# Kernel optimization log

Hardware: AMD Instinct MI355X
Metric: run time of the kernel (lower is better)

## Reference

```python
import jax, jax.numpy as jnp
import numpy as np

TEMPERATURE = 1.0

def _logic_layer(x, sel_a, sel_b, gate_logits, temp):
    # x: [B, in], sel_a/sel_b: [n, in], gate_logits: [n, 16]
    a = jax.nn.softmax(sel_a / temp, axis=-1)
    b = jax.nn.softmax(sel_b / temp, axis=-1)
    p = jnp.einsum('bi,ni->bn', x, a)  # first soft operand  [B, n]
    q = jnp.einsum('bi,ni->bn', x, b)  # second soft operand [B, n]
    pq = p * q
    one = jnp.ones_like(p)
    zero = jnp.zeros_like(p)
    # 16 two-input probabilistic logic gates (difflogic ordering)
    gates = jnp.stack([
        zero,               # FALSE
        pq,                 # AND
        p - pq,             # A AND NOT B
        p,                  # A
        q - pq,             # NOT A AND B
        q,                  # B
        p + q - 2 * pq,     # XOR
        p + q - pq,         # OR
        one - (p + q - pq), # NOR
        one - (p + q - 2 * pq),  # XNOR
        one - q,            # NOT B
        one - q + pq,       # A OR NOT B
        one - p,            # NOT A
        one - p + pq,       # NOT A OR B
        one - pq,           # NAND
        one,                # TRUE
    ], axis=-1)  # [B, n, 16]
    w = jax.nn.softmax(gate_logits / temp, axis=-1)  # [n, 16]
    return jnp.einsum('bng,ng->bn', gates, w)


def setup_inputs() -> dict:
    key = jax.random.key(0)
    ks = jax.random.split(key, 13)
    B = 1048576  # 1024x1024 CA grid, flattened cells
    inp = {'x': jax.random.uniform(ks[0], (B, 9), dtype=jnp.float32)}
    dims = [(8, 9), (4, 8), (2, 4), (1, 2)]
    i = 1
    for li, (n, d) in enumerate(dims, start=1):
        inp[f'sa{li}'] = jax.random.normal(ks[i], (n, d), dtype=jnp.float32); i += 1
        inp[f'sb{li}'] = jax.random.normal(ks[i], (n, d), dtype=jnp.float32); i += 1
        inp[f'g{li}'] = jax.random.normal(ks[i], (n, 16), dtype=jnp.float32); i += 1
    return inp


def reference(x, sa1, sb1, g1, sa2, sb2, g2, sa3, sb3, g3, sa4, sb4, g4):
    t = TEMPERATURE
    h = _logic_layer(x, sa1, sb1, g1, t)   # [B, 8]
    h = _logic_layer(h, sa2, sb2, g2, t)   # [B, 4]
    h = _logic_layer(h, sa3, sb3, g3, t)   # [B, 2]
    h = _logic_layer(h, sa4, sb4, g4, t)   # [B, 1]
    return h
```

## Files before the change

### kernel.cpp

```cpp
#include <hip/hip_runtime.h>
#include <math.h>


#define THREADS 256
#define SPT 4
#define B_PER_BLOCK (THREADS * SPT)

template <int D>
__device__ __forceinline__ void softmax_row(const float* __restrict__ src,
                                            float* __restrict__ dst) {
    float e[D];
    float m = src[0];
    #pragma unroll
    for (int i = 1; i < D; ++i) m = fmaxf(m, src[i]);
    float s = 0.f;
    #pragma unroll
    for (int i = 0; i < D; ++i) { e[i] = __expf(src[i] - m); s += e[i]; }
    float inv = 1.f / s;
    #pragma unroll
    for (int i = 0; i < D; ++i) dst[i] = e[i] * inv;
}

__device__ __forceinline__ void gate_fold(const float* __restrict__ g,
                                          float* __restrict__ C) {
    const float k0[16]  = {0,0,0,0, 0,0,0,0, 1, 1, 1, 1, 1, 1, 1, 1};
    const float kp[16]  = {0,0,1,1, 0,0,1,1,-1,-1, 0, 0,-1,-1, 0, 0};
    const float kq[16]  = {0,0,0,0, 1,1,1,1,-1,-1,-1,-1, 0, 0, 0, 0};
    const float kpq[16] = {0,1,-1,0,-1,0,-2,-1, 1, 2, 0, 1, 0, 1,-1, 0};
    float w[16];
    float m = g[0];
    #pragma unroll
    for (int i = 1; i < 16; ++i) m = fmaxf(m, g[i]);
    float s = 0.f;
    #pragma unroll
    for (int i = 0; i < 16; ++i) { w[i] = __expf(g[i] - m); s += w[i]; }
    float inv = 1.f / s;
    float c0 = 0, c1 = 0, c2 = 0, c3 = 0;
    #pragma unroll
    for (int i = 0; i < 16; ++i) {
        float wi = w[i] * inv;
        c0 = fmaf(wi, k0[i], c0); c1 = fmaf(wi, kp[i], c1);
        c2 = fmaf(wi, kq[i], c2); c3 = fmaf(wi, kpq[i], c3);
    }
    C[0] = c0; C[1] = c1; C[2] = c2; C[3] = c3;
}

__global__ void coeff_kernel(const float* __restrict__ sa1, const float* __restrict__ sb1, const float* __restrict__ g1,
                             const float* __restrict__ sa2, const float* __restrict__ sb2, const float* __restrict__ g2,
                             const float* __restrict__ sa3, const float* __restrict__ sb3, const float* __restrict__ g3,
                             const float* __restrict__ sa4, const float* __restrict__ sb4, const float* __restrict__ g4,
                             float* __restrict__ cf) {
    int t = threadIdx.x;
    if (t < 8) {
        int j = t;
        softmax_row<9>(sa1 + j * 9, cf + j * 9);
        softmax_row<9>(sb1 + j * 9, cf + 72 + j * 9);
        gate_fold(g1 + j * 16, cf + 144 + j * 4);
    } else if (t < 12) {
        int j = t - 8;
        softmax_row<8>(sa2 + j * 8, cf + 176 + j * 8);
        softmax_row<8>(sb2 + j * 8, cf + 208 + j * 8);
        gate_fold(g2 + j * 16, cf + 240 + j * 4);
    } else if (t < 14) {
        int j = t - 12;
        softmax_row<4>(sa3 + j * 4, cf + 256 + j * 4);
        softmax_row<4>(sb3 + j * 4, cf + 264 + j * 4);
        gate_fold(g3 + j * 16, cf + 272 + j * 4);
    } else if (t == 14) {
        softmax_row<2>(sa4, cf + 280);
        softmax_row<2>(sb4, cf + 282);
        gate_fold(g4, cf + 284);
    }
}

__global__ __launch_bounds__(THREADS, 3) void net_kernel(
        const float* __restrict__ x, const float* __restrict__ cf,
        float* __restrict__ out, int nB) {
    const int T  = blockIdx.x * THREADS + threadIdx.x;
    const int b0 = T * SPT;
    if (b0 >= nB) return;

    float v[SPT][9];
    if (b0 + SPT <= nB) {
        const float4* __restrict__ x4 = (const float4*)x;
        float4 r[9];
        #pragma unroll
        for (int k = 0; k < 9; ++k) r[k] = x4[(long)T * 9 + k];
        const float* rf = (const float*)r;
        #pragma unroll
        for (int s = 0; s < SPT; ++s)
            #pragma unroll
            for (int i = 0; i < 9; ++i) v[s][i] = rf[s * 9 + i];
    } else {
        #pragma unroll
        for (int s = 0; s < SPT; ++s)
            #pragma unroll
            for (int i = 0; i < 9; ++i) {
                int b = b0 + s;
                v[s][i] = (b < nB) ? x[(long)b * 9 + i] : 0.f;
            }
    }

    float h1[SPT][8];
    #pragma unroll
    for (int j = 0; j < 8; ++j) {
        #pragma unroll
        for (int s = 0; s < SPT; ++s) {
            float p = 0.f, q = 0.f;
            #pragma unroll
            for (int i = 0; i < 9; ++i) {
                p = fmaf(v[s][i], cf[     j * 9 + i], p);
                q = fmaf(v[s][i], cf[72 + j * 9 + i], q);
            }
            h1[s][j] = fmaf(cf[144 + j*4 + 3], p * q,
                       fmaf(cf[144 + j*4 + 2], q,
                       fmaf(cf[144 + j*4 + 1], p, cf[144 + j*4 + 0])));
        }
    }
    float h2[SPT][4];
    #pragma unroll
    for (int j = 0; j < 4; ++j) {
        #pragma unroll
        for (int s = 0; s < SPT; ++s) {
            float p = 0.f, q = 0.f;
            #pragma unroll
            for (int i = 0; i < 8; ++i) {
                p = fmaf(h1[s][i], cf[176 + j * 8 + i], p);
                q = fmaf(h1[s][i], cf[208 + j * 8 + i], q);
            }
            h2[s][j] = fmaf(cf[240 + j*4 + 3], p * q,
                       fmaf(cf[240 + j*4 + 2], q,
                       fmaf(cf[240 + j*4 + 1], p, cf[240 + j*4 + 0])));
        }
    }
    float h3[SPT][2];
    #pragma unroll
    for (int j = 0; j < 2; ++j) {
        #pragma unroll
        for (int s = 0; s < SPT; ++s) {
            float p = 0.f, q = 0.f;
            #pragma unroll
            for (int i = 0; i < 4; ++i) {
                p = fmaf(h2[s][i], cf[256 + j * 4 + i], p);
                q = fmaf(h2[s][i], cf[264 + j * 4 + i], q);
            }
            h3[s][j] = fmaf(cf[272 + j*4 + 3], p * q,
                       fmaf(cf[272 + j*4 + 2], q,
                       fmaf(cf[272 + j*4 + 1], p, cf[272 + j*4 + 0])));
        }
    }
    float o[SPT];
    #pragma unroll
    for (int s = 0; s < SPT; ++s) {
        float p = fmaf(h3[s][0], cf[280], h3[s][1] * cf[281]);
        float q = fmaf(h3[s][0], cf[282], h3[s][1] * cf[283]);
        o[s] = fmaf(cf[287], p * q,
               fmaf(cf[286], q,
               fmaf(cf[285], p, cf[284])));
    }
    if (b0 + SPT <= nB) {
        float4* __restrict__ out4 = (float4*)out;
        float4 w; w.x = o[0]; w.y = o[1]; w.z = o[2]; w.w = o[3];
        out4[T] = w;
    } else {
        #pragma unroll
        for (int s = 0; s < SPT; ++s)
            if (b0 + s < nB) out[b0 + s] = o[s];
    }
}

extern "C" void kernel_launch(void* const* d_in, const int* in_sizes, int n_in,
                              void* d_out, int out_size, void* d_ws, size_t ws_size,
                              hipStream_t stream) {
    const float* x   = (const float*)d_in[0];
    const float* sa1 = (const float*)d_in[1];
    const float* sb1 = (const float*)d_in[2];
    const float* g1  = (const float*)d_in[3];
    const float* sa2 = (const float*)d_in[4];
    const float* sb2 = (const float*)d_in[5];
    const float* g2  = (const float*)d_in[6];
    const float* sa3 = (const float*)d_in[7];
    const float* sb3 = (const float*)d_in[8];
    const float* g3  = (const float*)d_in[9];
    const float* sa4 = (const float*)d_in[10];
    const float* sb4 = (const float*)d_in[11];
    const float* g4  = (const float*)d_in[12];
    float* cf = (float*)d_ws;
    const int nB = in_sizes[0] / 9;

    coeff_kernel<<<1, 64, 0, stream>>>(sa1, sb1, g1, sa2, sb2, g2,
                                       sa3, sb3, g3, sa4, sb4, g4, cf);
    const int grid = (nB + B_PER_BLOCK - 1) / B_PER_BLOCK;
    net_kernel<<<grid, THREADS, 0, stream>>>(x, cf, (float*)d_out, nB);
}
```

Baseline: 107.6 us.

## Stage input tile through LDS for coalesced loads and strided sample mapping

The main kernel now loads each block's input tile into shared memory with fully coalesced float4 reads, then has each thread read 4 samples strided by the block width. The results are written back through shared memory so the output store stays a coalesced float4 write. Before, each thread loaded 9 consecutive float4s, so neighbouring lanes' accesses were 144 bytes apart. The change adds 36 KB of LDS per block and two extra barriers, which may limit occupancy. The coefficient kernel is also rebalanced so that more threads each compute one softmax row.

Result: slower. 113.6 us (+5.5%).

```diff
diff --git a/kernel.cpp b/kernel.cpp
--- a/kernel.cpp
+++ b/kernel.cpp
@@ -50,55 +50,62 @@
                              const float* __restrict__ sa3, const float* __restrict__ sb3, const float* __restrict__ g3,
                              const float* __restrict__ sa4, const float* __restrict__ sb4, const float* __restrict__ g4,
                              float* __restrict__ cf) {
-    int t = threadIdx.x;
-    if (t < 8) {
-        int j = t;
-        softmax_row<9>(sa1 + j * 9, cf + j * 9);
-        softmax_row<9>(sb1 + j * 9, cf + 72 + j * 9);
-        gate_fold(g1 + j * 16, cf + 144 + j * 4);
-    } else if (t < 12) {
-        int j = t - 8;
-        softmax_row<8>(sa2 + j * 8, cf + 176 + j * 8);
-        softmax_row<8>(sb2 + j * 8, cf + 208 + j * 8);
-        gate_fold(g2 + j * 16, cf + 240 + j * 4);
-    } else if (t < 14) {
-        int j = t - 12;
-        softmax_row<4>(sa3 + j * 4, cf + 256 + j * 4);
-        softmax_row<4>(sb3 + j * 4, cf + 264 + j * 4);
-        gate_fold(g3 + j * 16, cf + 272 + j * 4);
-    } else if (t == 14) {
-        softmax_row<2>(sa4, cf + 280);
-        softmax_row<2>(sb4, cf + 282);
-        gate_fold(g4, cf + 284);
+    const int t = threadIdx.x;
+    if (t < 15) {
+        int r = t;
+        if      (r < 8)  softmax_row<9>(sa1 + r * 9,        cf + r * 9);
+        else if (r < 12) softmax_row<8>(sa2 + (r - 8) * 8,  cf + 176 + (r - 8) * 8);
+        else if (r < 14) softmax_row<4>(sa3 + (r - 12) * 4, cf + 256 + (r - 12) * 4);
+        else             softmax_row<2>(sa4,                cf + 280);
+    } else if (t >= 16 && t < 31) {
+        int r = t - 16;
+        if      (r < 8)  softmax_row<9>(sb1 + r * 9,        cf + 72 + r * 9);
+        else if (r < 12) softmax_row<8>(sb2 + (r - 8) * 8,  cf + 208 + (r - 8) * 8);
+        else if (r < 14) softmax_row<4>(sb3 + (r - 12) * 4, cf + 264 + (r - 12) * 4);
+        else             softmax_row<2>(sb4,                cf + 282);
+    } else if (t >= 32 && t < 47) {
+        int r = t - 32;
+        if      (r < 8)  gate_fold(g1 + r * 16,        cf + 144 + r * 4);
+        else if (r < 12) gate_fold(g2 + (r - 8) * 16,  cf + 240 + (r - 8) * 4);
+        else if (r < 14) gate_fold(g3 + (r - 12) * 16, cf + 272 + (r - 12) * 4);
+        else             gate_fold(g4,                 cf + 284);
     }
 }
 
 __global__ __launch_bounds__(THREADS, 3) void net_kernel(
         const float* __restrict__ x, const float* __restrict__ cf,
         float* __restrict__ out, int nB) {
-    const int T  = blockIdx.x * THREADS + threadIdx.x;
-    const int b0 = T * SPT;
-    if (b0 >= nB) return;
+    __shared__ float sx[B_PER_BLOCK * 9];
+    const int t = threadIdx.x;
+    const int blockBase = blockIdx.x * B_PER_BLOCK;
+    const int total  = nB * 9;
+    const int f4base = blockBase * 9 / 4;
+
+    const float4* __restrict__ x4 = (const float4*)x;
+    float4* sx4 = (float4*)sx;
+    #pragma unroll
+    for (int k = 0; k < 9; ++k) {
+        int idx = t + k * THREADS;
+        int fi  = f4base + idx;
+        int e   = fi * 4;
+        if (e + 3 < total) {
+            sx4[idx] = x4[fi];
+        } else {
+            float4 vv = {0.f, 0.f, 0.f, 0.f};
+            if (e     < total) vv.x = x[e];
+            if (e + 1 < total) vv.y = x[e + 1];
+            if (e + 2 < total) vv.z = x[e + 2];
+            sx4[idx] = vv;
+        }
+    }
+    __syncthreads();
 
     float v[SPT][9];
-    if (b0 + SPT <= nB) {
-        const float4* __restrict__ x4 = (const float4*)x;
-        float4 r[9];
-        #pragma unroll
-        for (int k = 0; k < 9; ++k) r[k] = x4[(long)T * 9 + k];
-        const float* rf = (const float*)r;
-        #pragma unroll
-        for (int s = 0; s < SPT; ++s)
-            #pragma unroll
-            for (int i = 0; i < 9; ++i) v[s][i] = rf[s * 9 + i];
-    } else {
-        #pragma unroll
-        for (int s = 0; s < SPT; ++s)
-            #pragma unroll
-            for (int i = 0; i < 9; ++i) {
-                int b = b0 + s;
-                v[s][i] = (b < nB) ? x[(long)b * 9 + i] : 0.f;
-            }
+    #pragma unroll
+    for (int s = 0; s < SPT; ++s) {
+        const int r = s * THREADS + t;
+        #pragma unroll
+        for (int i = 0; i < 9; ++i) v[s][i] = sx[r * 9 + i];
     }
 
     float h1[SPT][8];
@@ -158,14 +165,19 @@
                fmaf(cf[286], q,
                fmaf(cf[285], p, cf[284])));
     }
+    const int b0 = blockBase + t * SPT;
+    __syncthreads();
+    #pragma unroll
+    for (int s = 0; s < SPT; ++s) sx[s * THREADS + t] = o[s];
+    __syncthreads();
     if (b0 + SPT <= nB) {
         float4* __restrict__ out4 = (float4*)out;
-        float4 w; w.x = o[0]; w.y = o[1]; w.z = o[2]; w.w = o[3];
-        out4[T] = w;
+        const float4* __restrict__ sxo = (const float4*)sx;
+        out4[blockBase / SPT + t] = sxo[t];
     } else {
         #pragma unroll
         for (int s = 0; s < SPT; ++s)
-            if (b0 + s < nB) out[b0 + s] = o[s];
+            if (b0 + s < nB) out[b0 + s] = sx[t * SPT + s];
     }
 }
 
```

## Fold coefficient softmax kernel into main kernel via shared memory

Applied to the files above, without the earlier changes.

Removes the separate single-block coefficient kernel and its workspace round-trip. Each wave of the main kernel now computes the softmaxed selector rows and folded gate coefficients into shared memory, then reads them from LDS instead of global memory. It also splits the first layer's loop into two chunks with a compiler memory barrier, likely to limit register pressure. In exchange, every wave redoes the exponentials, and the code has no __syncthreads, so it relies on wave-synchronous LDS visibility. Uniform LDS reads may also cost more than the scalar global loads they replace.

Result: slower. 144.5 us (+34.3%).

```diff
diff --git a/kernel.cpp b/kernel.cpp
--- a/kernel.cpp
+++ b/kernel.cpp
@@ -45,38 +45,39 @@
     C[0] = c0; C[1] = c1; C[2] = c2; C[3] = c3;
 }
 
-__global__ void coeff_kernel(const float* __restrict__ sa1, const float* __restrict__ sb1, const float* __restrict__ g1,
-                             const float* __restrict__ sa2, const float* __restrict__ sb2, const float* __restrict__ g2,
-                             const float* __restrict__ sa3, const float* __restrict__ sb3, const float* __restrict__ g3,
-                             const float* __restrict__ sa4, const float* __restrict__ sb4, const float* __restrict__ g4,
-                             float* __restrict__ cf) {
-    int t = threadIdx.x;
-    if (t < 8) {
-        int j = t;
-        softmax_row<9>(sa1 + j * 9, cf + j * 9);
-        softmax_row<9>(sb1 + j * 9, cf + 72 + j * 9);
-        gate_fold(g1 + j * 16, cf + 144 + j * 4);
-    } else if (t < 12) {
-        int j = t - 8;
-        softmax_row<8>(sa2 + j * 8, cf + 176 + j * 8);
-        softmax_row<8>(sb2 + j * 8, cf + 208 + j * 8);
-        gate_fold(g2 + j * 16, cf + 240 + j * 4);
-    } else if (t < 14) {
-        int j = t - 12;
-        softmax_row<4>(sa3 + j * 4, cf + 256 + j * 4);
-        softmax_row<4>(sb3 + j * 4, cf + 264 + j * 4);
-        gate_fold(g3 + j * 16, cf + 272 + j * 4);
-    } else if (t == 14) {
-        softmax_row<2>(sa4, cf + 280);
-        softmax_row<2>(sb4, cf + 282);
-        gate_fold(g4, cf + 284);
-    }
-}
-
 __global__ __launch_bounds__(THREADS, 3) void net_kernel(
-        const float* __restrict__ x, const float* __restrict__ cf,
+        const float* __restrict__ x,
+        const float* __restrict__ sa1, const float* __restrict__ sb1, const float* __restrict__ g1,
+        const float* __restrict__ sa2, const float* __restrict__ sb2, const float* __restrict__ g2,
+        const float* __restrict__ sa3, const float* __restrict__ sb3, const float* __restrict__ g3,
+        const float* __restrict__ sa4, const float* __restrict__ sb4, const float* __restrict__ g4,
         float* __restrict__ out, int nB) {
-    const int T  = blockIdx.x * THREADS + threadIdx.x;
+    __shared__ float scf[288];
+
+    const int t    = threadIdx.x;
+    const int lane = t & 63;
+
+    if (lane < 15) {
+        int r = lane;
+        if      (r < 8)  softmax_row<9>(sa1 + r * 9,        scf + r * 9);
+        else if (r < 12) softmax_row<8>(sa2 + (r - 8) * 8,  scf + 176 + (r - 8) * 8);
+        else if (r < 14) softmax_row<4>(sa3 + (r - 12) * 4, scf + 256 + (r - 12) * 4);
+        else             softmax_row<2>(sa4,                scf + 280);
+    } else if (lane >= 16 && lane < 31) {
+        int r = lane - 16;
+        if      (r < 8)  softmax_row<9>(sb1 + r * 9,        scf + 72 + r * 9);
+        else if (r < 12) softmax_row<8>(sb2 + (r - 8) * 8,  scf + 208 + (r - 8) * 8);
+        else if (r < 14) softmax_row<4>(sb3 + (r - 12) * 4, scf + 264 + (r - 12) * 4);
+        else             softmax_row<2>(sb4,                scf + 282);
+    } else if (lane >= 32 && lane < 47) {
+        int r = lane - 32;
+        if      (r < 8)  gate_fold(g1 + r * 16,        scf + 144 + r * 4);
+        else if (r < 12) gate_fold(g2 + (r - 8) * 16,  scf + 240 + (r - 8) * 4);
+        else if (r < 14) gate_fold(g3 + (r - 12) * 16, scf + 272 + (r - 12) * 4);
+        else             gate_fold(g4,                 scf + 284);
+    }
+
+    const int T  = blockIdx.x * THREADS + t;
     const int b0 = T * SPT;
     if (b0 >= nB) return;
 
@@ -103,60 +104,65 @@
 
     float h1[SPT][8];
     #pragma unroll
-    for (int j = 0; j < 8; ++j) {
+    for (int jc = 0; jc < 2; ++jc) {
+        #pragma unroll
+        for (int jj = 0; jj < 4; ++jj) {
+            const int j = jc * 4 + jj;
+            #pragma unroll
+            for (int s = 0; s < SPT; ++s) {
+                float p = 0.f, q = 0.f;
+                #pragma unroll
+                for (int i = 0; i < 9; ++i) {
+                    p = fmaf(v[s][i], scf[     j * 9 + i], p);
+                    q = fmaf(v[s][i], scf[72 + j * 9 + i], q);
+                }
+                h1[s][j] = fmaf(scf[144 + j*4 + 3], p * q,
+                           fmaf(scf[144 + j*4 + 2], q,
+                           fmaf(scf[144 + j*4 + 1], p, scf[144 + j*4 + 0])));
+            }
+        }
+        asm volatile("" ::: "memory");
+    }
+    float h2[SPT][4];
+    #pragma unroll
+    for (int j = 0; j < 4; ++j) {
         #pragma unroll
         for (int s = 0; s < SPT; ++s) {
             float p = 0.f, q = 0.f;
             #pragma unroll
-            for (int i = 0; i < 9; ++i) {
-                p = fmaf(v[s][i], cf[     j * 9 + i], p);
-                q = fmaf(v[s][i], cf[72 + j * 9 + i], q);
-            }
-            h1[s][j] = fmaf(cf[144 + j*4 + 3], p * q,
-                       fmaf(cf[144 + j*4 + 2], q,
-                       fmaf(cf[144 + j*4 + 1], p, cf[144 + j*4 + 0])));
+            for (int i = 0; i < 8; ++i) {
+                p = fmaf(h1[s][i], scf[176 + j * 8 + i], p);
+                q = fmaf(h1[s][i], scf[208 + j * 8 + i], q);
+            }
+            h2[s][j] = fmaf(scf[240 + j*4 + 3], p * q,
+                       fmaf(scf[240 + j*4 + 2], q,
+                       fmaf(scf[240 + j*4 + 1], p, scf[240 + j*4 + 0])));
         }
     }
-    float h2[SPT][4];
-    #pragma unroll
-    for (int j = 0; j < 4; ++j) {
+    float h3[SPT][2];
+    #pragma unroll
+    for (int j = 0; j < 2; ++j) {
         #pragma unroll
         for (int s = 0; s < SPT; ++s) {
             float p = 0.f, q = 0.f;
             #pragma unroll
-            for (int i = 0; i < 8; ++i) {
-                p = fmaf(h1[s][i], cf[176 + j * 8 + i], p);
-                q = fmaf(h1[s][i], cf[208 + j * 8 + i], q);
-            }
-            h2[s][j] = fmaf(cf[240 + j*4 + 3], p * q,
-                       fmaf(cf[240 + j*4 + 2], q,
-                       fmaf(cf[240 + j*4 + 1], p, cf[240 + j*4 + 0])));
+            for (int i = 0; i < 4; ++i) {
+                p = fmaf(h2[s][i], scf[256 + j * 4 + i], p);
+                q = fmaf(h2[s][i], scf[264 + j * 4 + i], q);
+            }
+            h3[s][j] = fmaf(scf[272 + j*4 + 3], p * q,
+                       fmaf(scf[272 + j*4 + 2], q,
+                       fmaf(scf[272 + j*4 + 1], p, scf[272 + j*4 + 0])));
         }
     }
-    float h3[SPT][2];
-    #pragma unroll
-    for (int j = 0; j < 2; ++j) {
-        #pragma unroll
-        for (int s = 0; s < SPT; ++s) {
-            float p = 0.f, q = 0.f;
-            #pragma unroll
-            for (int i = 0; i < 4; ++i) {
-                p = fmaf(h2[s][i], cf[256 + j * 4 + i], p);
-                q = fmaf(h2[s][i], cf[264 + j * 4 + i], q);
-            }
-            h3[s][j] = fmaf(cf[272 + j*4 + 3], p * q,
-                       fmaf(cf[272 + j*4 + 2], q,
-                       fmaf(cf[272 + j*4 + 1], p, cf[272 + j*4 + 0])));
-        }
-    }
     float o[SPT];
     #pragma unroll
     for (int s = 0; s < SPT; ++s) {
-        float p = fmaf(h3[s][0], cf[280], h3[s][1] * cf[281]);
-        float q = fmaf(h3[s][0], cf[282], h3[s][1] * cf[283]);
-        o[s] = fmaf(cf[287], p * q,
-               fmaf(cf[286], q,
-               fmaf(cf[285], p, cf[284])));
+        float p = fmaf(h3[s][0], scf[280], h3[s][1] * scf[281]);
+        float q = fmaf(h3[s][0], scf[282], h3[s][1] * scf[283]);
+        o[s] = fmaf(scf[287], p * q,
+               fmaf(scf[286], q,
+               fmaf(scf[285], p, scf[284])));
     }
     if (b0 + SPT <= nB) {
         float4* __restrict__ out4 = (float4*)out;
@@ -185,11 +191,10 @@
     const float* sa4 = (const float*)d_in[10];
     const float* sb4 = (const float*)d_in[11];
     const float* g4  = (const float*)d_in[12];
-    float* cf = (float*)d_ws;
     const int nB = in_sizes[0] / 9;
 
-    coeff_kernel<<<1, 64, 0, stream>>>(sa1, sb1, g1, sa2, sb2, g2,
-                                       sa3, sb3, g3, sa4, sb4, g4, cf);
     const int grid = (nB + B_PER_BLOCK - 1) / B_PER_BLOCK;
-    net_kernel<<<grid, THREADS, 0, stream>>>(x, cf, (float*)d_out, nB);
-}
+    net_kernel<<<grid, THREADS, 0, stream>>>(
+        x, sa1, sb1, g1, sa2, sb2, g2, sa3, sb3, g3, sa4, sb4, g4,
+        (float*)d_out, nB);
+}
```
